# Kernel tuning notes

Hardware: AMD Instinct MI355X
Metric: run time of the kernel (lower is better)

The kernel has to match this reference:

```python
import jax, jax.numpy as jnp
import numpy as np

B, N, D = 64, 576, 384   # batch, patches (24^2, perfect square), embed_dim
K = 4096                 # n_pairs
NUM_TARGETS = 2


def setup_inputs() -> dict:
    key = jax.random.key(0)
    k1, k2, k3, k4 = jax.random.split(key, 4)
    z = jax.random.normal(k1, (B, N, D), dtype=jnp.float32)
    indices = jax.random.randint(k2, (B, K, 2), 0, N, dtype=jnp.int64)
    W = jax.random.normal(k3, (NUM_TARGETS, 2 * D), dtype=jnp.float32) * (1.0 / np.sqrt(2 * D))
    bias = jax.random.normal(k4, (NUM_TARGETS,), dtype=jnp.float32) * 0.01
    return {"z": z, "indices": indices, "W": W, "bias": bias}


def reference(z, indices, W, bias):
    b, n, d = z.shape
    _, k, _ = indices.shape
    # index_pairs: per-batch gather of both pair members -> [b, k, 2, d]
    flat_idx = indices.reshape(b, k * 2)                      # [b, 2k]
    pairs = jnp.take_along_axis(z, flat_idx[:, :, None], axis=1)  # [b, 2k, d]
    pairs = pairs.reshape(b, k, 2 * d)                        # concat pair features
    # pairwise_mlp head: Linear(2d -> num_targets)
    out = jnp.einsum('bkf,tf->bkt', pairs, W) + bias          # [b, k, num_targets]
    return out, indices
```

## Files before the change

### kernel.cpp

```cpp
#include <hip/hip_runtime.h>
#include <hip/hip_bf16.h>

#define B_ 64
#define N_ 576
#define D_ 384
#define K_ 4096

__global__ __launch_bounds__(256) void partvit_proj(const float* __restrict__ z,
                                                    const float* __restrict__ W,
                                                    float* __restrict__ y) {
    const int wid  = (blockIdx.x * blockDim.x + threadIdx.x) >> 6;
    const int lane = threadIdx.x & 63;
    const int h = lane >> 5;
    const int s = lane & 31;

    const float4* Wq = reinterpret_cast<const float4*>(W);
    const float4* zq = reinterpret_cast<const float4*>(z);

    float4 w0a[3], w1a[3], w0b[3], w1b[3];
#pragma unroll
    for (int m = 0; m < 3; ++m) {
        const int c4 = s * 3 + m;
        w0a[m] = Wq[c4];
        w0b[m] = Wq[96 + c4];
        w1a[m] = Wq[192 + c4];
        w1b[m] = Wq[288 + c4];
    }

    const int npairs = (B_ * N_) / 2;
    const int nwaves = (gridDim.x * blockDim.x) >> 6;
    for (int pid = wid; pid < npairs; pid += nwaves) {
        const int row = pid * 2 + h;
        const float4* zr = zq + (size_t)row * 96 + s * 3;
        float a0 = 0.f, a1 = 0.f, a2 = 0.f, a3 = 0.f;
#pragma unroll
        for (int m = 0; m < 3; ++m) {
            const float4 v = zr[m];
            a0 += v.x * w0a[m].x + v.y * w0a[m].y + v.z * w0a[m].z + v.w * w0a[m].w;
            a1 += v.x * w1a[m].x + v.y * w1a[m].y + v.z * w1a[m].z + v.w * w1a[m].w;
            a2 += v.x * w0b[m].x + v.y * w0b[m].y + v.z * w0b[m].z + v.w * w0b[m].w;
            a3 += v.x * w1b[m].x + v.y * w1b[m].y + v.z * w1b[m].z + v.w * w1b[m].w;
        }
#pragma unroll
        for (int off = 16; off > 0; off >>= 1) {
            a0 += __shfl_xor(a0, off);
            a1 += __shfl_xor(a1, off);
            a2 += __shfl_xor(a2, off);
            a3 += __shfl_xor(a3, off);
        }
        if (s == 0) {
            float4 v;
            v.x = a0; v.y = a1; v.z = a2; v.w = a3;
            reinterpret_cast<float4*>(y)[row] = v;
        }
    }
}

__global__ __launch_bounds__(256) void partvit_gather(const int* __restrict__ idx,
                                                      const float* __restrict__ y,
                                                      const float* __restrict__ bias,
                                                      float* __restrict__ out,
                                                      float* __restrict__ idx_out) {
    const int t = blockIdx.x * blockDim.x + threadIdx.x;
    if (t >= B_ * K_) return;
    const int b = t >> 12;

    const int2 p = reinterpret_cast<const int2*>(idx)[t];
    const float* yb = y + (size_t)b * N_ * 4;

    const float2 y0 = *reinterpret_cast<const float2*>(yb + (size_t)p.x * 4);
    const float2 y1 = *reinterpret_cast<const float2*>(yb + (size_t)p.y * 4 + 2);

    const float b0 = bias[0], b1 = bias[1];

    float2 o;
    o.x = y0.x + y1.x + b0;
    o.y = y0.y + y1.y + b1;
    reinterpret_cast<float2*>(out)[t] = o;

    float2 io;
    io.x = (float)p.x;
    io.y = (float)p.y;
    reinterpret_cast<float2*>(idx_out)[t] = io;
}

extern "C" void kernel_launch(void* const* d_in, const int* in_sizes, int n_in,
                              void* d_out, int out_size, void* d_ws, size_t ws_size,
                              hipStream_t stream) {
    const float* z    = (const float*)d_in[0];
    const int*   idx  = (const int*)d_in[1];
    const float* W    = (const float*)d_in[2];
    const float* bias = (const float*)d_in[3];

    float* out     = (float*)d_out;
    float* idx_out = (float*)d_out + (size_t)B_ * K_ * 2;
    float* y       = (float*)d_ws;

    partvit_proj<<<1024, 256, 0, stream>>>(z, W, y);

    const int pairs = B_ * K_;
    partvit_gather<<<(pairs + 255) / 256, 256, 0, stream>>>(idx, y, bias, out, idx_out);
}
```

Measured before the change: 19.47 us.

## Fuse projection and gather into one kernel via per-batch last-block counter

Merges the row projection and pair-gather kernels into one launch. Each block projects a fixed slice of one batch's rows, then bumps an atomic per-batch counter, and the last block to finish performs that batch's gather. This removes the second kernel launch and the global barrier between stages, but adds a memset launch and atomics. The gather is now done by only 64 blocks, one per batch, which serializes that work into a small tail.

```diff
diff --git a/kernel.cpp b/kernel.cpp
--- a/kernel.cpp
+++ b/kernel.cpp
@@ -5,18 +5,25 @@
 #define N_ 576
 #define D_ 384
 #define K_ 4096
+#define BLOCKS_PER_BATCH 16
+#define ROWS_PER_BLOCK (N_ / BLOCKS_PER_BATCH)
 
-__global__ __launch_bounds__(256) void partvit_proj(const float* __restrict__ z,
-                                                    const float* __restrict__ W,
-                                                    float* __restrict__ y) {
-    const int wid  = (blockIdx.x * blockDim.x + threadIdx.x) >> 6;
-    const int lane = threadIdx.x & 63;
-    const int h = lane >> 5;
-    const int s = lane & 31;
+__global__ __launch_bounds__(256) void partvit_fused(const float* __restrict__ z,
+                                                     const int* __restrict__ idx,
+                                                     const float* __restrict__ W,
+                                                     const float* __restrict__ bias,
+                                                     float* __restrict__ out,
+                                                     float* __restrict__ idx_out,
+                                                     float* __restrict__ y,
+                                                     unsigned int* __restrict__ ctr) {
+    const int g = blockIdx.x;
+    const int b = g >> 4;
+    const int c = g & 15;
+    const int tid = threadIdx.x;
+    const int hw = tid >> 5;
+    const int s  = tid & 31;
 
     const float4* Wq = reinterpret_cast<const float4*>(W);
-    const float4* zq = reinterpret_cast<const float4*>(z);
-
     float4 w0a[3], w1a[3], w0b[3], w1b[3];
 #pragma unroll
     for (int m = 0; m < 3; ++m) {
@@ -27,10 +34,11 @@
         w1b[m] = Wq[288 + c4];
     }
 
-    const int npairs = (B_ * N_) / 2;
-    const int nwaves = (gridDim.x * blockDim.x) >> 6;
-    for (int pid = wid; pid < npairs; pid += nwaves) {
-        const int row = pid * 2 + h;
+    const int row0 = b * N_ + c * ROWS_PER_BLOCK;
+    const float4* zq = reinterpret_cast<const float4*>(z);
+
+    for (int r = hw; r < ROWS_PER_BLOCK; r += 8) {
+        const int row = row0 + r;
         const float4* zr = zq + (size_t)row * 96 + s * 3;
         float a0 = 0.f, a1 = 0.f, a2 = 0.f, a3 = 0.f;
 #pragma unroll
@@ -54,34 +62,35 @@
             reinterpret_cast<float4*>(y)[row] = v;
         }
     }
-}
 
-__global__ __launch_bounds__(256) void partvit_gather(const int* __restrict__ idx,
-                                                      const float* __restrict__ y,
-                                                      const float* __restrict__ bias,
-                                                      float* __restrict__ out,
-                                                      float* __restrict__ idx_out) {
-    const int t = blockIdx.x * blockDim.x + threadIdx.x;
-    if (t >= B_ * K_) return;
-    const int b = t >> 12;
+    __shared__ unsigned int old_s;
+    __syncthreads();
+    if (tid == 0) {
+        __threadfence();
+        old_s = atomicAdd(&ctr[b], 1u);
+    }
+    __syncthreads();
+    if (old_s != BLOCKS_PER_BATCH - 1) return;
 
-    const int2 p = reinterpret_cast<const int2*>(idx)[t];
-    const float* yb = y + (size_t)b * N_ * 4;
-
-    const float2 y0 = *reinterpret_cast<const float2*>(yb + (size_t)p.x * 4);
-    const float2 y1 = *reinterpret_cast<const float2*>(yb + (size_t)p.y * 4 + 2);
+    __threadfence();
 
     const float b0 = bias[0], b1 = bias[1];
-
-    float2 o;
-    o.x = y0.x + y1.x + b0;
-    o.y = y0.y + y1.y + b1;
-    reinterpret_cast<float2*>(out)[t] = o;
-
-    float2 io;
-    io.x = (float)p.x;
-    io.y = (float)p.y;
-    reinterpret_cast<float2*>(idx_out)[t] = io;
+    const float* yb = y + (size_t)b * N_ * 4;
+    const int base = b * K_;
+    for (int i = tid; i < K_; i += 256) {
+        const int t = base + i;
+        const int2 p = reinterpret_cast<const int2*>(idx)[t];
+        const float2 y0 = *reinterpret_cast<const float2*>(yb + (size_t)p.x * 4);
+        const float2 y1 = *reinterpret_cast<const float2*>(yb + (size_t)p.y * 4 + 2);
+        float2 o;
+        o.x = y0.x + y1.x + b0;
+        o.y = y0.y + y1.y + b1;
+        reinterpret_cast<float2*>(out)[t] = o;
+        float2 io;
+        io.x = (float)p.x;
+        io.y = (float)p.y;
+        reinterpret_cast<float2*>(idx_out)[t] = io;
+    }
 }
 
 extern "C" void kernel_launch(void* const* d_in, const int* in_sizes, int n_in,
@@ -95,9 +104,10 @@
     float* out     = (float*)d_out;
     float* idx_out = (float*)d_out + (size_t)B_ * K_ * 2;
     float* y       = (float*)d_ws;
+    unsigned int* ctr = (unsigned int*)((char*)d_ws + (1 << 20));
 
-    partvit_proj<<<1024, 256, 0, stream>>>(z, W, y);
+    hipMemsetAsync(ctr, 0, B_ * sizeof(unsigned int), stream);
 
-    const int pairs = B_ * K_;
-    partvit_gather<<<(pairs + 255) / 256, 256, 0, stream>>>(idx, y, bias, out, idx_out);
+    partvit_fused<<<B_ * BLOCKS_PER_BATCH, 256, 0, stream>>>(z, idx, W, bias,
+                                                             out, idx_out, y, ctr);
 }
```

Result: slower. 73.52 us (+277.5%).
